# Optimization experiments

Hardware: AMD Instinct MI355X
Metric: run time of the kernel (lower is better)

The kernel has to match this reference:

```python
import jax, jax.numpy as jnp
import numpy as np

DIM_D = 32
DIM_J = 32
DIM_X = 2 * DIM_D + 1  # 65: (dim_d+1) vd slice + dim_d C_R slice
DIM_H = 256
N = 100
DT = 0.01
JUMP_P = 0.05  # per-step jump probability
BATCH = 4096


def setup_inputs() -> dict:
    key = jax.random.key(0)
    ks = jax.random.split(key, 8)

    def he(k, shape):  # kaiming_normal_, fan_in mode (matches torch init)
        return (jax.random.normal(k, shape, dtype=jnp.float32)
                * jnp.sqrt(2.0 / shape[1]))

    W1 = he(ks[0], (DIM_H, DIM_X + 1))
    W2 = he(ks[1], (DIM_H, DIM_H))
    W3 = he(ks[2], (DIM_H, DIM_H))
    W4 = he(ks[3], (DIM_D, DIM_H))
    b1 = jnp.zeros((DIM_H,), jnp.float32)
    b2 = jnp.zeros((DIM_H,), jnp.float32)
    b3 = jnp.zeros((DIM_H,), jnp.float32)
    b4 = jnp.zeros((DIM_D,), jnp.float32)
    # x_0 in (0, 0.5) so -log(1 - x) is well defined; s, d positive rates
    x_0 = jax.random.uniform(ks[4], (DIM_X,), jnp.float32, 0.05, 0.5)
    s = jax.random.uniform(ks[5], (DIM_D, 1), jnp.float32, 0.5, 1.5)
    d_param = jax.random.uniform(ks[6], (1,), jnp.float32, 0.5, 1.5)
    return {"W1": W1, "b1": b1, "W2": W2, "b2": b2, "W3": W3, "b3": b3,
            "W4": W4, "b4": b4, "x_0": x_0, "s": s, "d_param": d_param,
            "batch_size": BATCH}


def _forward(W1, b1, W2, b2, W3, b3, W4, b4, x_0, s, d_param, batch_size):
    B = batch_size

    def phi(z):  # 4-layer MLP: relu x3 -> sigmoid, control in (0,1)^dim_d
        z = jax.nn.relu(z @ W1.T + b1)
        z = jax.nn.relu(z @ W2.T + b2)
        z = jax.nn.relu(z @ W3.T + b3)
        return jax.nn.sigmoid(z @ W4.T + b4)

    x0 = jnp.broadcast_to(x_0.astype(jnp.float32), (B, DIM_X))
    h_V0 = -jnp.log(1.0 - x0[:, :DIM_D]) / s[:, 0]          # [B, D]
    h_D0 = x0[:, DIM_D:DIM_D + 1] / d_param[0]              # [B, 1]
    h0 = jnp.concatenate([h_V0, h_D0], axis=-1)             # [B, D+1]
    CR0 = x0[:, -DIM_D:]                                    # [B, D]
    f0 = jnp.zeros((B, 1), jnp.float32)
    base_key = jax.random.key(1234)

    def step(carry, n):
        x, h, C_R, f = carry
        t = DT * n.astype(jnp.float32)
        time = jnp.ones((B, 1), jnp.float32) * t
        control = phi(jnp.concatenate([x, time], axis=-1))  # [B, D]
        k = jax.random.fold_in(base_key, n)
        jumps = jax.random.bernoulli(k, JUMP_P, (B, DIM_J)).astype(jnp.float32)
        # running cost f += f(t, x) * dt
        f = f + jnp.sum(x[:, :DIM_D], axis=-1, keepdims=True) * DT
        # step_forward: hazard clocks advance by dt, jump resets V-clocks
        hV = jnp.where(jumps > 0, 0.0, h[:, :DIM_D] + DT)
        hD = h[:, DIM_D:] + DT
        h_new = jnp.concatenate([hV, hD], axis=-1)
        # dCR: cumulative reward driven by control at jump times
        C_R_new = C_R + control * jumps
        # h_to_vd: invert the h_V / h_D maps
        V = 1.0 - jnp.exp(-s[:, 0] * hV)                     # [B, D]
        Dv = d_param[0] * hD                                 # [B, 1]
        x_new = jnp.concatenate([V, Dv, C_R_new], axis=-1)   # [B, 2D+1]
        return (x_new, h_new, C_R_new, f), (control, x_new)

    (x_last, _, _, f), (controls, xs) = jax.lax.scan(
        step, (x0, h0, CR0, f0), jnp.arange(N - 1))
    # control_tensor[:, n] filled for n < N-1, last row stays zero (as in torch)
    control_tensor = jnp.concatenate(
        [jnp.swapaxes(controls, 0, 1), jnp.zeros((B, 1, DIM_D), jnp.float32)],
        axis=1)                                              # [B, N, D]
    x_tensor = jnp.concatenate(
        [x0[:, None, :], jnp.swapaxes(xs, 0, 1)], axis=1)    # [B, N, 2D+1]
    # J = f + g(x, poiss); g = terminal value of cumulative reward slice
    J = f + jnp.sum(x_last[:, -DIM_D:], axis=-1, keepdims=True)
    return control_tensor, x_tensor, J[:, :, None]


def reference(W1, b1, W2, b2, W3, b3, W4, b4, x_0, s, d_param, batch_size):
    return _forward(W1, b1, W2, b2, W3, b3, W4, b4, x_0, s, d_param,
                    int(batch_size))
```

## Files before the change

kernel.cpp:

```cpp
#include <hip/hip_runtime.h>
#include <cstdint>
#include <cstddef>

#define DIM_D 32
#define KIN   66
#define DIM_H 256
#define NSTE  100
#define BATCHN 4096
#define ROWS  16
#define BLKT  512
#define NBLK  (BATCHN / ROWS)

#define CTRL_OFF 0
#define X_OFF ((size_t)BATCHN * NSTE * DIM_D)
#define J_OFF (X_OFF + (size_t)BATCHN * NSTE * 65)

#define W1B_OFF 0
#define W2B_OFF 24576
#define W3B_OFF 90112
#define W4B_OFF 155648
#define WS_ELEMS 163840

constexpr float DT_C = 0.01f;

typedef __bf16 bf16x8 __attribute__((ext_vector_type(8)));
typedef float  f32x4  __attribute__((ext_vector_type(4)));

__device__ __forceinline__ uint32_t rotl32(uint32_t x, int n) {
  return (x << n) | (x >> (32 - n));
}

__device__ __forceinline__ void tf2x32(uint32_t k0, uint32_t k1,
                                       uint32_t x0, uint32_t x1,
                                       uint32_t& o0, uint32_t& o1) {
  uint32_t k2 = k0 ^ k1 ^ 0x1BD11BDAu;
#define TFR(r) { x0 += x1; x1 = rotl32(x1, (r)); x1 ^= x0; }
  x0 += k0; x1 += k1;
  TFR(13) TFR(15) TFR(26) TFR(6)   x0 += k1; x1 += k2 + 1u;
  TFR(17) TFR(29) TFR(16) TFR(24)  x0 += k2; x1 += k0 + 2u;
  TFR(13) TFR(15) TFR(26) TFR(6)   x0 += k0; x1 += k1 + 3u;
  TFR(17) TFR(29) TFR(16) TFR(24)  x0 += k1; x1 += k2 + 4u;
  TFR(13) TFR(15) TFR(26) TFR(6)   x0 += k2; x1 += k0 + 5u;
#undef TFR
  o0 = x0; o1 = x1;
}

__global__ void conv_w(const float* __restrict__ W1, const float* __restrict__ W2,
                       const float* __restrict__ W3, const float* __restrict__ W4,
                       __bf16* __restrict__ ws) {
  int t = blockIdx.x * 256 + threadIdx.x;
  if (t < W2B_OFF) {
    int r = t / 96, c = t % 96;
    ws[t] = (c < KIN) ? (__bf16)W1[r * KIN + c] : (__bf16)0.0f;
  } else if (t < W3B_OFF) {
    ws[t] = (__bf16)W2[t - W2B_OFF];
  } else if (t < W4B_OFF) {
    ws[t] = (__bf16)W3[t - W3B_OFF];
  } else if (t < WS_ELEMS) {
    ws[t] = (__bf16)W4[t - W4B_OFF];
  }
}

__device__ __forceinline__ f32x4 mfma16(bf16x8 a, bf16x8 b, f32x4 c) {
  return __builtin_amdgcn_mfma_f32_16x16x32_bf16(a, b, c, 0, 0, 0);
}

__device__ __forceinline__ int swz256(int row, int col) { return row * 256 + (col ^ ((row & 15) << 4)); }
__device__ __forceinline__ int swz512(int row, int col) { return row * 512 + (col ^ ((row & 15) << 4)); }

__global__ __launch_bounds__(BLKT, 2) void model_kernel(
    const __bf16* __restrict__ ws,
    const float* __restrict__ b1, const float* __restrict__ b2,
    const float* __restrict__ b3, const float* __restrict__ b4,
    const float* __restrict__ x0p, const float* __restrict__ sp,
    const float* __restrict__ dpp, float* __restrict__ out)
{
  __shared__ __bf16 xb[ROWS * 128];
  __shared__ __bf16 actA[ROWS * 256];
  __shared__ __bf16 actB[ROWS * 256];
  __shared__ float  psum[8][16][16];
  __shared__ float  xVf[ROWS][DIM_D];
  __shared__ float  crf[ROWS][DIM_D];
  __shared__ float  hVl[ROWS][DIM_D];
  __shared__ float  hDl[ROWS], fl[ROWS];
  __shared__ float  s_sh[DIM_D];
  __shared__ float  dp_sh;
  __shared__ uint32_t keys[NSTE - 1][2];

  const int tid = threadIdx.x;
  const int r0  = blockIdx.x * ROWS;
  char* xbB = (char*)xb;
  char* aAB = (char*)actA;
  char* aBB = (char*)actB;

  if (tid < NSTE - 1) {
    uint32_t o0, o1;
    tf2x32(0u, 1234u, 0u, (uint32_t)tid, o0, o1);
    keys[tid][0] = o0; keys[tid][1] = o1;
  }
  if (tid < DIM_D) s_sh[tid] = sp[tid];
  if (tid == 0)    dp_sh = dpp[0];
  for (int i = tid; i < ROWS * 128; i += BLKT) xb[i] = (__bf16)0.0f;
  __syncthreads();

  for (int i = tid; i < ROWS * KIN; i += BLKT) {
    int r = i / KIN, c = i % KIN;
    float v = (c < 65) ? x0p[c] : 0.0f;
    *(__bf16*)(xbB + swz256(r, c * 2)) = (__bf16)v;
    if (c < 65) out[X_OFF + (size_t)(r0 + r) * NSTE * 65 + c] = v;
  }
  for (int i = tid; i < ROWS * DIM_D; i += BLKT) {
    int r = i / DIM_D, d = i % DIM_D;
    xVf[r][d] = x0p[d];
    crf[r][d] = x0p[33 + d];
    hVl[r][d] = -logf(1.0f - x0p[d]) / s_sh[d];
    out[CTRL_OFF + (size_t)(r0 + r) * NSTE * DIM_D + (size_t)(NSTE - 1) * DIM_D + d] = 0.0f;
  }
  if (tid < ROWS) { hDl[tid] = x0p[DIM_D] / dp_sh; fl[tid] = 0.0f; }

  const int wv = tid >> 6;
  const int ln = tid & 63;
  const int lr = ln & 15;
  const int g  = ln >> 4;
  const int lk8 = g * 8;

  bf16x8 w1f[2][3], w2f[2][8], w3f[2][8], w4f[2];
#pragma unroll
  for (int t = 0; t < 2; ++t) {
    const int n1 = wv * 32 + t * 16 + lr;
#pragma unroll
    for (int ks = 0; ks < 3; ++ks)
      w1f[t][ks] = *(const bf16x8*)(ws + W1B_OFF + n1 * 96 + ks * 32 + lk8);
#pragma unroll
    for (int ks = 0; ks < 8; ++ks) {
      w2f[t][ks] = *(const bf16x8*)(ws + W2B_OFF + n1 * 256 + ks * 32 + lk8);
      w3f[t][ks] = *(const bf16x8*)(ws + W3B_OFF + n1 * 256 + ks * 32 + lk8);
    }
  }
  {
    const int t4 = wv >> 2, kc = wv & 3;
#pragma unroll
    for (int ks2 = 0; ks2 < 2; ++ks2)
      w4f[ks2] = *(const bf16x8*)(ws + W4B_OFF + (t4 * 16 + lr) * 256 + (kc * 2 + ks2) * 32 + lk8);
  }
  const float bb1_0 = b1[wv * 32 + lr], bb1_1 = b1[wv * 32 + 16 + lr];
  const float bb2_0 = b2[wv * 32 + lr], bb2_1 = b2[wv * 32 + 16 + lr];
  const float bb3_0 = b3[wv * 32 + lr], bb3_1 = b3[wv * 32 + 16 + lr];
  const float b4d = b4[tid & 31];
  const int er = tid >> 5, ed = tid & 31;
  __syncthreads();

  for (int n = 0; n < NSTE - 1; ++n) {
    {
      f32x4 a0 = {bb1_0, bb1_0, bb1_0, bb1_0};
      f32x4 a1 = {bb1_1, bb1_1, bb1_1, bb1_1};
#pragma unroll
      for (int ks = 0; ks < 3; ++ks) {
        bf16x8 af = *(const bf16x8*)(xbB + swz256(lr, ks * 64 + g * 16));
        a0 = mfma16(af, w1f[0][ks], a0);
        a1 = mfma16(af, w1f[1][ks], a1);
      }
#pragma unroll
      for (int q = 0; q < 4; ++q) {
        int row = g * 4 + q;
        *(__bf16*)(aAB + swz512(row, (wv * 32 + lr) * 2))      = (__bf16)fmaxf(a0[q], 0.0f);
        *(__bf16*)(aAB + swz512(row, (wv * 32 + 16 + lr) * 2)) = (__bf16)fmaxf(a1[q], 0.0f);
      }
    }
    __syncthreads();
    {
      f32x4 a0 = {bb2_0, bb2_0, bb2_0, bb2_0};
      f32x4 a1 = {bb2_1, bb2_1, bb2_1, bb2_1};
#pragma unroll
      for (int ks = 0; ks < 8; ++ks) {
        bf16x8 af = *(const bf16x8*)(aAB + swz512(lr, ks * 64 + g * 16));
        a0 = mfma16(af, w2f[0][ks], a0);
        a1 = mfma16(af, w2f[1][ks], a1);
      }
#pragma unroll
      for (int q = 0; q < 4; ++q) {
        int row = g * 4 + q;
        *(__bf16*)(aBB + swz512(row, (wv * 32 + lr) * 2))      = (__bf16)fmaxf(a0[q], 0.0f);
        *(__bf16*)(aBB + swz512(row, (wv * 32 + 16 + lr) * 2)) = (__bf16)fmaxf(a1[q], 0.0f);
      }
    }
    __syncthreads();
    {
      f32x4 a0 = {bb3_0, bb3_0, bb3_0, bb3_0};
      f32x4 a1 = {bb3_1, bb3_1, bb3_1, bb3_1};
#pragma unroll
      for (int ks = 0; ks < 8; ++ks) {
        bf16x8 af = *(const bf16x8*)(aBB + swz512(lr, ks * 64 + g * 16));
        a0 = mfma16(af, w3f[0][ks], a0);
        a1 = mfma16(af, w3f[1][ks], a1);
      }
#pragma unroll
      for (int q = 0; q < 4; ++q) {
        int row = g * 4 + q;
        *(__bf16*)(aAB + swz512(row, (wv * 32 + lr) * 2))      = (__bf16)fmaxf(a0[q], 0.0f);
        *(__bf16*)(aAB + swz512(row, (wv * 32 + 16 + lr) * 2)) = (__bf16)fmaxf(a1[q], 0.0f);
      }
    }
    __syncthreads();
    {
      const int kc = wv & 3;
      f32x4 a4 = {0.0f, 0.0f, 0.0f, 0.0f};
#pragma unroll
      for (int ks2 = 0; ks2 < 2; ++ks2) {
        const int ks = kc * 2 + ks2;
        bf16x8 af = *(const bf16x8*)(aAB + swz512(lr, ks * 64 + g * 16));
        a4 = mfma16(af, w4f[ks2], a4);
      }
#pragma unroll
      for (int q = 0; q < 4; ++q) psum[wv][g * 4 + q][lr] = a4[q];
    }
    if (tid < ROWS) {
      float s = 0.0f;
#pragma unroll
      for (int d = 0; d < DIM_D; ++d) s += xVf[tid][d];
      fl[tid] += s * DT_C;
    }
    __syncthreads();
    {
      const int r = er, d = ed;
      float up = b4d;
      const int g0 = (d >> 4) * 4, c = d & 15;
#pragma unroll
      for (int w2 = 0; w2 < 4; ++w2) up += psum[g0 + w2][r][c];
      const float u = 1.0f / (1.0f + expf(-up));
      out[CTRL_OFF + (size_t)(r0 + r) * NSTE * DIM_D + (size_t)n * DIM_D + d] = u;

      const uint32_t F = (uint32_t)((r0 + r) * DIM_D + d);
      uint32_t o0, o1;
      tf2x32(keys[n][0], keys[n][1], 0u, F, o0, o1);
      const uint32_t bits = o0 ^ o1;
      const float uf = __uint_as_float((bits >> 9) | 0x3f800000u) - 1.0f;
      const bool jump = uf < 0.05f;

      float hv = jump ? 0.0f : (hVl[r][d] + DT_C);
      hVl[r][d] = hv;
      float cr = crf[r][d] + (jump ? u : 0.0f);
      crf[r][d] = cr;
      float V = 1.0f - expf(-s_sh[d] * hv);
      xVf[r][d] = V;

      const size_t xo = X_OFF + (size_t)(r0 + r) * NSTE * 65 + (size_t)(n + 1) * 65;
      out[xo + d] = V;
      out[xo + 33 + d] = cr;
      *(__bf16*)(xbB + swz256(r, d * 2))        = (__bf16)V;
      *(__bf16*)(xbB + swz256(r, (33 + d) * 2)) = (__bf16)cr;
      if (d == 0) {
        float hd = hDl[r] + DT_C; hDl[r] = hd;
        float Dv = dp_sh * hd;
        out[xo + 32] = Dv;
        *(__bf16*)(xbB + swz256(r, 64))  = (__bf16)Dv;
        *(__bf16*)(xbB + swz256(r, 130)) = (__bf16)(DT_C * (float)(n + 1));
      }
    }
    __syncthreads();
  }

  if (tid < ROWS) {
    float s = 0.0f;
#pragma unroll
    for (int d = 0; d < DIM_D; ++d) s += crf[tid][d];
    out[J_OFF + (size_t)(r0 + tid)] = fl[tid] + s;
  }
}

extern "C" void kernel_launch(void* const* d_in, const int* in_sizes, int n_in,
                              void* d_out, int out_size, void* d_ws, size_t ws_size,
                              hipStream_t stream) {
  const float* W1 = (const float*)d_in[0];
  const float* b1 = (const float*)d_in[1];
  const float* W2 = (const float*)d_in[2];
  const float* b2 = (const float*)d_in[3];
  const float* W3 = (const float*)d_in[4];
  const float* b3 = (const float*)d_in[5];
  const float* W4 = (const float*)d_in[6];
  const float* b4 = (const float*)d_in[7];
  const float* x0 = (const float*)d_in[8];
  const float* s  = (const float*)d_in[9];
  const float* dp = (const float*)d_in[10];
  __bf16* ws = (__bf16*)d_ws;
  float* out = (float*)d_out;

  hipLaunchKernelGGL(conv_w, dim3(WS_ELEMS / 256), dim3(256), 0, stream, W1, W2, W3, W4, ws);
  hipLaunchKernelGGL(model_kernel, dim3(NBLK), dim3(BLKT), 0, stream,
                     ws, b1, b2, b3, b4, x0, s, dp, out);
}
```

Measured before the change: 260.4 us.

## Halve rows per block and precompute jump masks with ballot before scan

Cuts rows per block from 16 to 8, doubling the block count to spread the serial 99-step recurrence over more CUs. The Threefry jump bits for all steps are computed up front (one wave per row, ballot into a 32-bit mask in shared memory), which takes the RNG off the per-step critical path. The cost is that MFMA tiles now carry only 8 useful rows out of 16, so half of each matrix op is wasted, and weights are reloaded into registers by twice as many blocks.

```diff
diff --git a/kernel.cpp b/kernel.cpp
--- a/kernel.cpp
+++ b/kernel.cpp
@@ -4,10 +4,9 @@
 
 #define DIM_D 32
 #define KIN   66
-#define DIM_H 256
 #define NSTE  100
 #define BATCHN 4096
-#define ROWS  16
+#define ROWS  8
 #define BLKT  512
 #define NBLK  (BATCHN / ROWS)
 
@@ -51,7 +50,7 @@
   int t = blockIdx.x * 256 + threadIdx.x;
   if (t < W2B_OFF) {
     int r = t / 96, c = t % 96;
-    ws[t] = (c < KIN) ? (__bf16)W1[r * KIN + c] : (__bf16)0.0f;
+    ws[t] = (c < KIN) ? (__bf16)W1[r * 66 + c] : (__bf16)0.0f;
   } else if (t < W3B_OFF) {
     ws[t] = (__bf16)W2[t - W2B_OFF];
   } else if (t < W4B_OFF) {
@@ -68,16 +67,16 @@
 __device__ __forceinline__ int swz256(int row, int col) { return row * 256 + (col ^ ((row & 15) << 4)); }
 __device__ __forceinline__ int swz512(int row, int col) { return row * 512 + (col ^ ((row & 15) << 4)); }
 
-__global__ __launch_bounds__(BLKT, 2) void model_kernel(
+__global__ void __launch_bounds__(BLKT, 2) model_kernel(
     const __bf16* __restrict__ ws,
     const float* __restrict__ b1, const float* __restrict__ b2,
     const float* __restrict__ b3, const float* __restrict__ b4,
     const float* __restrict__ x0p, const float* __restrict__ sp,
     const float* __restrict__ dpp, float* __restrict__ out)
 {
-  __shared__ __bf16 xb[ROWS * 128];
-  __shared__ __bf16 actA[ROWS * 256];
-  __shared__ __bf16 actB[ROWS * 256];
+  __shared__ __bf16 xb[16 * 128];
+  __shared__ __bf16 actA[16 * 256];
+  __shared__ __bf16 actB[16 * 256];
   __shared__ float  psum[8][16][16];
   __shared__ float  xVf[ROWS][DIM_D];
   __shared__ float  crf[ROWS][DIM_D];
@@ -86,6 +85,7 @@
   __shared__ float  s_sh[DIM_D];
   __shared__ float  dp_sh;
   __shared__ uint32_t keys[NSTE - 1][2];
+  __shared__ uint32_t jb[NSTE - 1][ROWS];
 
   const int tid = threadIdx.x;
   const int r0  = blockIdx.x * ROWS;
@@ -100,8 +100,26 @@
   }
   if (tid < DIM_D) s_sh[tid] = sp[tid];
   if (tid == 0)    dp_sh = dpp[0];
-  for (int i = tid; i < ROWS * 128; i += BLKT) xb[i] = (__bf16)0.0f;
+  for (int i = tid; i < 16 * 128; i += BLKT) xb[i] = (__bf16)0.0f;
   __syncthreads();
+
+  const int wv = tid >> 6;
+  const int ln = tid & 63;
+  const int lr = ln & 15;
+  const int g  = ln >> 4;
+  const int lk8 = g * 8;
+
+  {
+    const uint32_t F = (uint32_t)((r0 + wv) * DIM_D + (ln & 31));
+    for (int n = 0; n < NSTE - 1; ++n) {
+      uint32_t o0, o1;
+      tf2x32(keys[n][0], keys[n][1], 0u, F, o0, o1);
+      const uint32_t bits = o0 ^ o1;
+      const float uf = __uint_as_float((bits >> 9) | 0x3f800000u) - 1.0f;
+      const unsigned long long m = __ballot(uf < 0.05f);
+      if (ln == 0) jb[n][wv] = (uint32_t)m;
+    }
+  }
 
   for (int i = tid; i < ROWS * KIN; i += BLKT) {
     int r = i / KIN, c = i % KIN;
@@ -118,12 +136,6 @@
   }
   if (tid < ROWS) { hDl[tid] = x0p[DIM_D] / dp_sh; fl[tid] = 0.0f; }
 
-  const int wv = tid >> 6;
-  const int ln = tid & 63;
-  const int lr = ln & 15;
-  const int g  = ln >> 4;
-  const int lk8 = g * 8;
-
   bf16x8 w1f[2][3], w2f[2][8], w3f[2][8], w4f[2];
 #pragma unroll
   for (int t = 0; t < 2; ++t) {
@@ -147,7 +159,6 @@
   const float bb2_0 = b2[wv * 32 + lr], bb2_1 = b2[wv * 32 + 16 + lr];
   const float bb3_0 = b3[wv * 32 + lr], bb3_1 = b3[wv * 32 + 16 + lr];
   const float b4d = b4[tid & 31];
-  const int er = tid >> 5, ed = tid & 31;
   __syncthreads();
 
   for (int n = 0; n < NSTE - 1; ++n) {
@@ -215,14 +226,14 @@
       for (int q = 0; q < 4; ++q) psum[wv][g * 4 + q][lr] = a4[q];
     }
     if (tid < ROWS) {
-      float s = 0.0f;
-#pragma unroll
-      for (int d = 0; d < DIM_D; ++d) s += xVf[tid][d];
-      fl[tid] += s * DT_C;
-    }
-    __syncthreads();
-    {
-      const int r = er, d = ed;
+      float sum = 0.0f;
+#pragma unroll
+      for (int d = 0; d < DIM_D; ++d) sum += xVf[tid][d];
+      fl[tid] += sum * DT_C;
+    }
+    __syncthreads();
+    if (tid < 256) {
+      const int r = tid >> 5, d = tid & 31;
       float up = b4d;
       const int g0 = (d >> 4) * 4, c = d & 15;
 #pragma unroll
@@ -230,13 +241,7 @@
       const float u = 1.0f / (1.0f + expf(-up));
       out[CTRL_OFF + (size_t)(r0 + r) * NSTE * DIM_D + (size_t)n * DIM_D + d] = u;
 
-      const uint32_t F = (uint32_t)((r0 + r) * DIM_D + d);
-      uint32_t o0, o1;
-      tf2x32(keys[n][0], keys[n][1], 0u, F, o0, o1);
-      const uint32_t bits = o0 ^ o1;
-      const float uf = __uint_as_float((bits >> 9) | 0x3f800000u) - 1.0f;
-      const bool jump = uf < 0.05f;
-
+      const bool jump = (jb[n][r] >> d) & 1;
       float hv = jump ? 0.0f : (hVl[r][d] + DT_C);
       hVl[r][d] = hv;
       float cr = crf[r][d] + (jump ? u : 0.0f);
```

Measured after the change: 501.0 us. 92.4% more time.
